# Performance work log

Measured on AMD Instinct MI355X. Metric: run time of the kernel, lower is better.

## Reference

```python
import jax, jax.numpy as jnp
import numpy as np

EPS_BN = 1e-5
EPS_NORM = 1e-12
TEMPERATURE = 0.1
TEMPLATE_LAMBDA = 0.5
KERNEL_WIDTH = 5


def conv1d(x, w, b, pad):
    # x: (B, Cin, W), w: (Cout, Cin, K)
    y = jax.lax.conv_general_dilated(x, w, window_strides=(1,), padding=[(pad, pad)],
                                     dimension_numbers=('NCW', 'OIW', 'NCW'))
    return y + b[None, :, None]


def batchnorm(x, g, be):
    # training-mode BN: batch stats over (B, W), biased variance (as torch)
    m = jnp.mean(x, axis=(0, 2), keepdims=True)
    v = jnp.mean((x - m) ** 2, axis=(0, 2), keepdims=True)
    return g[None, :, None] * (x - m) * jax.lax.rsqrt(v + EPS_BN) + be[None, :, None]


def maxpool4(x):
    return jax.lax.reduce_window(x, -jnp.inf, jax.lax.max, (1, 1, 4), (1, 1, 4), 'VALID')


def adaptive_avg_pool1d(x, k):
    # faithful torch AdaptiveAvgPool1d bin boundaries
    W = x.shape[-1]
    outs = []
    for i in range(k):
        s = (i * W) // k
        e = -(-((i + 1) * W) // k)  # ceil
        outs.append(jnp.mean(x[..., s:e], axis=-1))
    return jnp.stack(outs, axis=-1)


def l2norm(x):
    n = jnp.linalg.norm(x, axis=-1, keepdims=True)
    return x / jnp.maximum(n, EPS_NORM)


def encoder(x, w1, b1, g1, be1, w2, b2, g2, be2, w3, b3, g3, be3):
    h = maxpool4(jax.nn.relu(batchnorm(conv1d(x, w1, b1, 8), g1, be1)))
    h = maxpool4(jax.nn.relu(batchnorm(conv1d(h, w2, b2, 8), g2, be2)))
    h = maxpool4(jax.nn.relu(batchnorm(conv1d(h, w3, b3, 8), g3, be3)))
    return h  # (B, C, W=L/64)


def template_head(h, tw1, tb1, tg1, tbe1, tw2, tb2, tg2, tbe2):
    k = jax.nn.relu(batchnorm(conv1d(h, tw1, tb1, 2), tg1, tbe1))
    k = jax.nn.relu(batchnorm(conv1d(k, tw2, tb2, 1), tg2, tbe2))
    return adaptive_avg_pool1d(k, KERNEL_WIDTH)  # (B, C, W_k)


def template_similarity(k, h):
    # Equivalent to the torch B*B*C grouped 'same' conv1d followed by
    # sum over channels and mean over positions: since the result is the
    # SUM over all output positions of a zero-padded cross-correlation,
    # it factorizes as einsum of k with shifted window-sums of h.
    k = k - jnp.mean(k, axis=-1, keepdims=True)
    k = l2norm(k)  # (B, C, Wk)
    h = h - jnp.mean(h, axis=-1, keepdims=True)
    h = l2norm(h)  # (B, C, W)
    Wk = k.shape[-1]
    W = h.shape[-1]
    pad = (Wk - 1) // 2  # padding='same' for odd kernel
    hp = jnp.pad(h, ((0, 0), (0, 0), (pad, pad)))
    # S[j,c,t] = sum_w hp[j,c,w+t]  for t in [0, Wk)
    S = jnp.stack([jnp.sum(hp[:, :, t:t + W], axis=-1) for t in range(Wk)], axis=-1)
    return jnp.einsum('ick,jck->ij', k, S) / W  # (B, B)


def infonce(sim):
    logp = jax.nn.log_softmax(sim / TEMPERATURE, axis=-1)
    return -jnp.mean(jnp.diagonal(logp))


def template_contrastive_loss(k1, k2):
    B = k1.shape[0]
    a = l2norm(k1.reshape(B, -1))
    b = l2norm(k2.reshape(B, -1))
    return infonce(jnp.matmul(a, b.T) * TEMPERATURE / TEMPERATURE) if False else infonce(jnp.matmul(a, b.T))


def setup_inputs() -> dict:
    key = jax.random.key(0)
    ks = jax.random.split(key, 12)
    B, L, C = 256, 8192, 64
    inp = {
        'x1': jax.random.normal(ks[0], (B, 1, L), dtype=jnp.float32),
        'x2': jax.random.normal(ks[1], (B, 1, L), dtype=jnp.float32),
        # encoder params
        'w1': jax.random.normal(ks[2], (16, 1, 17), dtype=jnp.float32) * 0.1,
        'b1': jnp.zeros((16,), jnp.float32),
        'g1': jnp.ones((16,), jnp.float32), 'be1': jnp.zeros((16,), jnp.float32),
        'w2': jax.random.normal(ks[3], (32, 16, 17), dtype=jnp.float32) * 0.05,
        'b2': jnp.zeros((32,), jnp.float32),
        'g2': jnp.ones((32,), jnp.float32), 'be2': jnp.zeros((32,), jnp.float32),
        'w3': jax.random.normal(ks[4], (C, 32, 17), dtype=jnp.float32) * 0.04,
        'b3': jnp.zeros((C,), jnp.float32),
        'g3': jnp.ones((C,), jnp.float32), 'be3': jnp.zeros((C,), jnp.float32),
        # template head params
        'tw1': jax.random.normal(ks[5], (C, C, 5), dtype=jnp.float32) * 0.05,
        'tb1': jnp.zeros((C,), jnp.float32),
        'tg1': jnp.ones((C,), jnp.float32), 'tbe1': jnp.zeros((C,), jnp.float32),
        'tw2': jax.random.normal(ks[6], (C, C, 3), dtype=jnp.float32) * 0.07,
        'tb2': jnp.zeros((C,), jnp.float32),
        'tg2': jnp.ones((C,), jnp.float32), 'tbe2': jnp.zeros((C,), jnp.float32),
    }
    return inp


def reference(x1, x2, w1, b1, g1, be1, w2, b2, g2, be2, w3, b3, g3, be3,
              tw1, tb1, tg1, tbe1, tw2, tb2, tg2, tbe2):
    enc = (w1, b1, g1, be1, w2, b2, g2, be2, w3, b3, g3, be3)
    th = (tw1, tb1, tg1, tbe1, tw2, tb2, tg2, tbe2)
    h1 = encoder(x1, *enc)
    h2 = encoder(x2, *enc)
    k1 = template_head(h1, *th)
    k2 = template_head(h2, *th)
    loss_matching = (infonce(template_similarity(k1, h2)) +
                     infonce(template_similarity(k2, h1))) / 2
    loss_template = template_contrastive_loss(k1, k2)
    return loss_matching + TEMPLATE_LAMBDA * loss_template
```

## Files before the change

### kernel.cpp

```cpp
#include <hip/hip_runtime.h>
#include <hip/hip_bf16.h>
#include <math.h>


#define BSZ2 512
#define NTHR 256

typedef __attribute__((ext_vector_type(8))) short bf16x8;
typedef __attribute__((ext_vector_type(4))) float f32x4;

static inline int ceil_divll(long long a, int b) { return (int)((a + b - 1) / b); }

__device__ __forceinline__ unsigned short f2bf(float f) {
    unsigned u = __float_as_uint(f);
    u = (u + 0x7FFFu + ((u >> 16) & 1u)) >> 16;
    return (unsigned short)u;
}
__device__ __forceinline__ float bf2f(unsigned short h) {
    return __uint_as_float(((unsigned)h) << 16);
}
__device__ __forceinline__ float bflo(unsigned u) { return __uint_as_float(u << 16); }
__device__ __forceinline__ float bfhi(unsigned u) { return __uint_as_float(u & 0xFFFF0000u); }

template<int WT, int MODE>
__global__ __launch_bounds__(256)
void conv1_mfma(const float* __restrict__ x1, const float* __restrict__ x2,
                const unsigned short* __restrict__ wpack1, const float* __restrict__ bias,
                const float* __restrict__ scale, const float* __restrict__ shift,
                unsigned short* __restrict__ out, float* __restrict__ partials)
{
    constexpr int W = 8192;
    constexpr int CHUNK = 4 * WT * 16;
    __shared__ float xs[CHUNK + 32];
    __shared__ float sred[(MODE == 0) ? 4 : 1][16];
    __shared__ float ssred[(MODE == 0) ? 4 : 1][16];

    const int tid = threadIdx.x;
    const int ntile = W / CHUNK;
    const int b = blockIdx.x / ntile;
    const int w0 = (blockIdx.x % ntile) * CHUNK;
    const float* xrow = (b < 256) ? x1 + (long long)b * W : x2 + (long long)(b - 256) * W;

    for (int i = tid; i < CHUNK + 32; i += 256) {
        const int gw = w0 - 8 + i;
        xs[i] = (gw >= 0 && gw < W) ? xrow[gw] : 0.f;
    }
    __syncthreads();

    const int lane = tid & 63, wave = tid >> 6;
    const int n = lane & 15, kq = lane >> 4;
    const bf16x8 a = *(const bf16x8*)(wpack1 + lane * 8);

    f32x4 acc[WT];
#pragma unroll
    for (int wt = 0; wt < WT; ++wt) { acc[wt][0]=0.f; acc[wt][1]=0.f; acc[wt][2]=0.f; acc[wt][3]=0.f; }

    const int base0 = wave * WT * 16 + n + kq * 8;
#pragma unroll
    for (int wt = 0; wt < WT; ++wt) {
        bf16x8 bv;
#pragma unroll
        for (int j = 0; j < 8; ++j) {
            __hip_bfloat16 h = __float2bfloat16(xs[base0 + wt * 16 + j]);
            bv[j] = *reinterpret_cast<short*>(&h);
        }
        acc[wt] = __builtin_amdgcn_mfma_f32_16x16x32_bf16(bv, a, acc[wt], 0, 0, 0);
    }

    if (MODE == 0) {
        const float bi = bias[n];
        float s_ = 0.f, ss_ = 0.f;
#pragma unroll
        for (int wt = 0; wt < WT; ++wt)
#pragma unroll
            for (int e = 0; e < 4; ++e) {
                const float y = acc[wt][e] + bi;
                s_ += y; ss_ += y * y;
            }
        s_  += __shfl_xor(s_, 16, 64);  s_  += __shfl_xor(s_, 32, 64);
        ss_ += __shfl_xor(ss_, 16, 64); ss_ += __shfl_xor(ss_, 32, 64);
        if (lane < 16) { sred[wave][n] = s_; ssred[wave][n] = ss_; }
        __syncthreads();
        if (tid < 16) {
            float sumv = 0.f, sumsq = 0.f;
#pragma unroll
            for (int wv = 0; wv < 4; ++wv) { sumv += sred[wv][tid]; sumsq += ssred[wv][tid]; }
            partials[((long long)blockIdx.x * 16 + tid) * 2 + 0] = sumv;
            partials[((long long)blockIdx.x * 16 + tid) * 2 + 1] = sumsq;
        }
    } else {
        const int half = b >> 8;
        const float bi = bias[n];
        const float scv = scale[half * 16 + n];
        const float shv = shift[half * 16 + n];
#pragma unroll
        for (int wt = 0; wt < WT; ++wt) {
            float v[4];
#pragma unroll
            for (int e = 0; e < 4; ++e) v[e] = fmaf(scv, acc[wt][e] + bi, shv);
            const float mx = fmaxf(fmaxf(fmaxf(v[0], v[1]), fmaxf(v[2], v[3])), 0.f);
            const int wp = (w0 >> 2) + wave * WT * 4 + wt * 4 + kq;
            out[((long long)b * 2048 + wp) * 16 + n] = f2bf(mx);
        }
    }
}

template<int COUT>
__global__ void finalize2(const float* __restrict__ partials, int nblk_half, float invN,
                          const float* __restrict__ g, const float* __restrict__ be,
                          float* __restrict__ scale, float* __restrict__ shift)
{
    const int co = blockIdx.x;
    const int half = blockIdx.y;
    const float* P = partials + (size_t)half * nblk_half * COUT * 2;
    float s = 0.f, ss = 0.f;
    for (int i = threadIdx.x; i < nblk_half; i += NTHR) {
        s  += P[((long long)i * COUT + co) * 2 + 0];
        ss += P[((long long)i * COUT + co) * 2 + 1];
    }
    __shared__ float red[NTHR][2];
    red[threadIdx.x][0] = s; red[threadIdx.x][1] = ss;
    __syncthreads();
    for (int off = NTHR / 2; off > 0; off >>= 1) {
        if ((int)threadIdx.x < off) {
            red[threadIdx.x][0] += red[threadIdx.x + off][0];
            red[threadIdx.x][1] += red[threadIdx.x + off][1];
        }
        __syncthreads();
    }
    if (threadIdx.x == 0) {
        const float m = red[0][0] * invN;
        const float v = red[0][1] * invN - m * m;
        const float inv = rsqrtf(v + 1e-5f);
        const float sc = g[co] * inv;
        scale[half * COUT + co] = sc;
        shift[half * COUT + co] = be[co] - sc * m;
    }
}

template<int CIN, int KK, int DT, int NP, int S, int CT>
__device__ __forceinline__ void pack_one(int idx, const float* __restrict__ wgt,
                                         unsigned short* __restrict__ wp)
{
    const int j = idx & 7;
    const int l = (idx >> 3) & 63;
    int rest = idx >> 9;
    const int ct = rest % CT; rest /= CT;
    const int s = rest % S;
    const int p = rest / S;
    const int co = ct * 16 + (l & 15);
    const int k = (l >> 4) * 8 + j;
    int ci, t;
    if (DT == 2) { ci = k & (CIN - 1); t = p * 2 + (k >> 4); }
    else         { ci = s * 32 + k;    t = p; }
    float v = (t < KK) ? wgt[((long long)co * CIN + ci) * KK + t] : 0.f;
    wp[idx] = f2bf(v);
}

__global__ void build_all_wpacks(const float* __restrict__ w1, const float* __restrict__ w2,
                                 const float* __restrict__ w3,
                                 const float* __restrict__ tw1, const float* __restrict__ tw2,
                                 unsigned short* __restrict__ wp1,
                                 unsigned short* __restrict__ wp2, unsigned short* __restrict__ wp3,
                                 unsigned short* __restrict__ wpt1, unsigned short* __restrict__ wpt2)
{
    const int idx = blockIdx.x * NTHR + threadIdx.x;
    const int n1 = 512;
    const int n2 = 9 * 1 * 2 * 512;
    const int n3 = 17 * 1 * 4 * 512;
    const int nt1 = 5 * 2 * 4 * 512;
    const int nt2 = 3 * 2 * 4 * 512;
    if (idx < n1) {
        const int j = idx & 7, l = idx >> 3;
        const int co = l & 15, k = (l >> 4) * 8 + j;
        wp1[idx] = f2bf((k < 17) ? w1[co * 17 + k] : 0.f);
    }
    else if (idx < n1 + n2) pack_one<16, 17, 2, 9, 1, 2>(idx - n1, w2, wp2);
    else if (idx < n1 + n2 + n3) pack_one<32, 17, 1, 17, 1, 4>(idx - n1 - n2, w3, wp3);
    else if (idx < n1 + n2 + n3 + nt1) pack_one<64, 5, 1, 5, 2, 4>(idx - n1 - n2 - n3, tw1, wpt1);
    else if (idx < n1 + n2 + n3 + nt1 + nt2) pack_one<64, 3, 1, 3, 2, 4>(idx - n1 - n2 - n3 - nt1, tw2, wpt2);
}

template<int CIN, int COUT, int KK, int PAD, int DT, int NP, int S, int CT, int ST,
         int SRCM, int OUTM>
__global__ __launch_bounds__(256)
void conv_mfma2(const unsigned short* __restrict__ xA, const unsigned short* __restrict__ xB,
                const float* __restrict__ pscale, const float* __restrict__ pshift,
                const unsigned short* __restrict__ wpack, const float* __restrict__ bias,
                unsigned short* __restrict__ outA, unsigned short* __restrict__ outB,
                float* __restrict__ partials, int W)
{
    constexpr int CHUNK = 4 * ST * 16;
    constexpr int ROWB = CIN * 2 + 16;
    constexpr int ROWS = CHUNK + KK + (DT - 1) + 1;
    constexpr int DPR = CIN / 2;
    __shared__ __align__(16) unsigned char lx[ROWS * ROWB];
    __shared__ float sred[4][CT][16];
    __shared__ float ssred[4][CT][16];
    __shared__ float scb[(SRCM > 0) ? CIN : 1];
    __shared__ float shb[(SRCM > 0) ? CIN : 1];

    const int tid = threadIdx.x;
    const int ntile = W / CHUNK;
    const int b = blockIdx.x / ntile;
    const int tile = blockIdx.x % ntile;
    const int w0 = tile * CHUNK;

    if (SRCM > 0) {
        if (tid < CIN) {
            scb[tid] = pscale[(b >> 8) * CIN + tid];
            shb[tid] = pshift[(b >> 8) * CIN + tid];
        }
        __syncthreads();
    }

    for (int d = tid; d < ROWS * DPR; d += 256) {
        const int row = d / DPR;
        const int col = d % DPR;
        const int gw = w0 - PAD + row;
        unsigned v = 0;
        if (gw >= 0 && gw < W) {
            const long long src = ((long long)b * W + gw) * CIN + col * 2;
            if (SRCM == 0) {
                v = *(const unsigned*)(xA + src);
            } else {
                const unsigned va = *(const unsigned*)(xA + src);
                const float sc0 = scb[col * 2], sh0 = shb[col * 2];
                const float sc1 = scb[col * 2 + 1], sh1 = shb[col * 2 + 1];
                float f0, f1;
                if (SRCM == 1) {
                    const unsigned vb = *(const unsigned*)(xB + src);
                    f0 = fmaxf(fmaf(sc0, (sc0 > 0.f) ? bflo(va) : bflo(vb), sh0), 0.f);
                    f1 = fmaxf(fmaf(sc1, (sc1 > 0.f) ? bfhi(va) : bfhi(vb), sh1), 0.f);
                } else {
                    f0 = fmaxf(fmaf(sc0, bflo(va), sh0), 0.f);
                    f1 = fmaxf(fmaf(sc1, bfhi(va), sh1), 0.f);
                }
                v = (unsigned)f2bf(f0) | ((unsigned)f2bf(f1) << 16);
            }
        }
        *(unsigned*)(lx + row * ROWB + col * 4) = v;
    }
    __syncthreads();

    const int lane = tid & 63, wave = tid >> 6;
    const int n = lane & 15, kq = lane >> 4;
    int rowbase, cbyte;
    if (DT == 2) { rowbase = wave * ST * 16 + n + (kq >> 1); cbyte = (kq & 1) * 16; }
    else         { rowbase = wave * ST * 16 + n;             cbyte = kq * 16; }

    f32x4 acc[ST][CT];
#pragma unroll
    for (int st = 0; st < ST; ++st)
#pragma unroll
        for (int ct = 0; ct < CT; ++ct) { acc[st][ct][0]=0.f; acc[st][ct][1]=0.f; acc[st][ct][2]=0.f; acc[st][ct][3]=0.f; }

#pragma unroll
    for (int p = 0; p < NP; ++p) {
#pragma unroll
        for (int s = 0; s < S; ++s) {
            bf16x8 a[CT];
#pragma unroll
            for (int ct = 0; ct < CT; ++ct)
                a[ct] = *(const bf16x8*)(wpack + (((long long)(p * S + s) * CT + ct) * 64 + lane) * 8);
#pragma unroll
            for (int st = 0; st < ST; ++st) {
                const int r = rowbase + st * 16 + p * DT;
                const bf16x8 bf = *(const bf16x8*)(lx + r * ROWB + cbyte + s * 64);
#pragma unroll
                for (int ct = 0; ct < CT; ++ct)
                    acc[st][ct] = __builtin_amdgcn_mfma_f32_16x16x32_bf16(bf, a[ct], acc[st][ct], 0, 0, 0);
            }
        }
    }

    float s_[CT], ss_[CT];
#pragma unroll
    for (int ct = 0; ct < CT; ++ct) { s_[ct] = 0.f; ss_[ct] = 0.f; }

#pragma unroll
    for (int st = 0; st < ST; ++st) {
        const int wbase = w0 + wave * ST * 16 + st * 16 + kq * 4;
#pragma unroll
        for (int ct = 0; ct < CT; ++ct) {
            const float bi = bias[ct * 16 + n];
            float v[4];
#pragma unroll
            for (int e = 0; e < 4; ++e) {
                v[e] = acc[st][ct][e] + bi;
                s_[ct] += v[e];
                ss_[ct] += v[e] * v[e];
            }
            if (OUTM == 0) {
#pragma unroll
                for (int e = 0; e < 4; ++e)
                    outA[((long long)b * W + wbase + e) * COUT + ct * 16 + n] = f2bf(v[e]);
            } else {
                const float mx = fmaxf(fmaxf(v[0], v[1]), fmaxf(v[2], v[3]));
                const float mn = fminf(fminf(v[0], v[1]), fminf(v[2], v[3]));
                const long long o = ((long long)b * (W >> 2) + (wbase >> 2)) * COUT + ct * 16 + n;
                outA[o] = f2bf(mx);
                outB[o] = f2bf(mn);
            }
        }
    }
#pragma unroll
    for (int ct = 0; ct < CT; ++ct) {
        s_[ct]  += __shfl_xor(s_[ct], 16, 64);  s_[ct]  += __shfl_xor(s_[ct], 32, 64);
        ss_[ct] += __shfl_xor(ss_[ct], 16, 64); ss_[ct] += __shfl_xor(ss_[ct], 32, 64);
    }
    if (lane < 16) {
#pragma unroll
        for (int ct = 0; ct < CT; ++ct) { sred[wave][ct][n] = s_[ct]; ssred[wave][ct][n] = ss_[ct]; }
    }
    __syncthreads();
    if (tid < COUT) {
        const int ct = tid >> 4, nn = tid & 15;
        float sumv = 0.f, sumsq = 0.f;
#pragma unroll
        for (int wv = 0; wv < 4; ++wv) { sumv += sred[wv][ct][nn]; sumsq += ssred[wv][ct][nn]; }
        partials[((long long)blockIdx.x * COUT + tid) * 2 + 0] = sumv;
        partials[((long long)blockIdx.x * COUT + tid) * 2 + 1] = sumsq;
    }
}

__global__ void tail_pool_srow(const unsigned short* __restrict__ yT2b,
                               const float* __restrict__ scT2, const float* __restrict__ shT2,
                               const unsigned short* __restrict__ yMax3,
                               const unsigned short* __restrict__ yMin3,
                               const float* __restrict__ scS3, const float* __restrict__ shS3,
                               float* __restrict__ kn, float* __restrict__ ab,
                               float* __restrict__ Sv)
{
    __shared__ float hb[128][64];
    const int tid = threadIdx.x;
    if (blockIdx.x < BSZ2) {
        const int b = blockIdx.x;
        __shared__ float pk[320];
        __shared__ float red2[NTHR];
        const uint2* yd = (const uint2*)(yT2b + (long long)b * 128 * 64);
        for (int i = tid; i < 128 * 16; i += 256) {
            const int w = i >> 4, c4 = (i & 15) * 4;
            const float* scp = scT2 + (b >> 8) * 64 + c4;
            const float* shp = shT2 + (b >> 8) * 64 + c4;
            const uint2 v = yd[i];
            hb[w][c4 + 0] = fmaxf(fmaf(scp[0], bflo(v.x), shp[0]), 0.f);
            hb[w][c4 + 1] = fmaxf(fmaf(scp[1], bfhi(v.x), shp[1]), 0.f);
            hb[w][c4 + 2] = fmaxf(fmaf(scp[2], bflo(v.y), shp[2]), 0.f);
            hb[w][c4 + 3] = fmaxf(fmaf(scp[3], bfhi(v.y), shp[3]), 0.f);
        }
        __syncthreads();
        const int bs[5] = {0, 25, 51, 76, 102};
        const int be[5] = {26, 52, 77, 103, 128};
        for (int o = tid; o < 320; o += 256) {
            const int cc = o & 63, bin = o >> 6;
            float acc = 0.f;
            for (int w = bs[bin]; w < be[bin]; ++w) acc += hb[w][cc];
            pk[cc * 5 + bin] = acc / (float)(be[bin] - bs[bin]);
        }
        __syncthreads();
        float n2p = pk[tid] * pk[tid];
        if (tid < 64) n2p += pk[256 + tid] * pk[256 + tid];
        red2[tid] = n2p;
        __syncthreads();
        for (int off = NTHR / 2; off > 0; off >>= 1) {
            if (tid < off) red2[tid] += red2[tid + off];
            __syncthreads();
        }
        const float nrm = fmaxf(sqrtf(red2[0]), 1e-12f);
        for (int i = tid; i < 320; i += 256) ab[(long long)b * 320 + i] = pk[i] / nrm;
        if (tid < 64) {
            const float* p = pk + tid * 5;
            float m = 0.f;
            for (int t = 0; t < 5; ++t) m += p[t];
            m *= 0.2f;
            float v[5]; float q = 0.f;
            for (int t = 0; t < 5; ++t) { v[t] = p[t] - m; q += v[t] * v[t]; }
            const float n = fmaxf(sqrtf(q), 1e-12f);
            float* o = kn + ((long long)b * 64 + tid) * 5;
            for (int t = 0; t < 5; ++t) o[t] = v[t] / n;
        }
    } else {
        __shared__ float red[4][64];
        __shared__ float mrow[64];
        const int b = blockIdx.x - BSZ2;
        const int c = tid & 63, grp = tid >> 6;
        const uint2* ya = (const uint2*)(yMax3 + (long long)b * 128 * 64);
        const uint2* yb = (const uint2*)(yMin3 + (long long)b * 128 * 64);
        for (int i = tid; i < 128 * 16; i += 256) {
            const int w = i >> 4, c4 = (i & 15) * 4;
            const float* scp = scS3 + (b >> 8) * 64 + c4;
            const float* shp = shS3 + (b >> 8) * 64 + c4;
            const uint2 va = ya[i], vb = yb[i];
            hb[w][c4 + 0] = fmaxf(fmaf(scp[0], (scp[0] > 0.f) ? bflo(va.x) : bflo(vb.x), shp[0]), 0.f);
            hb[w][c4 + 1] = fmaxf(fmaf(scp[1], (scp[1] > 0.f) ? bfhi(va.x) : bfhi(vb.x), shp[1]), 0.f);
            hb[w][c4 + 2] = fmaxf(fmaf(scp[2], (scp[2] > 0.f) ? bflo(va.y) : bflo(vb.y), shp[2]), 0.f);
            hb[w][c4 + 3] = fmaxf(fmaf(scp[3], (scp[3] > 0.f) ? bfhi(va.y) : bfhi(vb.y), shp[3]), 0.f);
        }
        __syncthreads();
        float s = 0.f;
        for (int w = grp * 32; w < grp * 32 + 32; ++w) s += hb[w][c];
        red[grp][c] = s;
        __syncthreads();
        if (tid < 64) mrow[tid] = (red[0][tid] + red[1][tid] + red[2][tid] + red[3][tid]) / 128.f;
        __syncthreads();
        const float m = mrow[c];
        float q = 0.f;
        for (int w = grp * 32; w < grp * 32 + 32; ++w) { const float d = hb[w][c] - m; q += d * d; }
        red[grp][c] = q;
        __syncthreads();
        if (tid < 64) {
            const float n2 = red[0][tid] + red[1][tid] + red[2][tid] + red[3][tid];
            const float n = fmaxf(sqrtf(n2), 1e-12f);
            const float m0 = mrow[tid];
            const float h0 = (hb[0][tid] - m0) / n, h1 = (hb[1][tid] - m0) / n;
            const float hN1 = (hb[127][tid] - m0) / n, hN2 = (hb[126][tid] - m0) / n;
            float* o = Sv + ((long long)b * 64 + tid) * 5;
            o[0] = -(hN2 + hN1); o[1] = -hN1; o[2] = 0.f; o[3] = -h0; o[4] = -(h0 + h1);
        }
    }
}

__global__ void simdot_nce(const float* __restrict__ kn, const float* __restrict__ Sv,
                           const float* __restrict__ ab, float* __restrict__ lp)
{
    const int j = threadIdx.x;
    const int i = blockIdx.x;
    const int z = blockIdx.y;
    const float* a;
    const float* b;
    float coef;
    if (z == 0)      { a = kn + (long long)i * 320;         b = Sv + (long long)(256 + j) * 320; coef = 10.f / 128.f; }
    else if (z == 1) { a = kn + (long long)(256 + i) * 320; b = Sv + (long long)j * 320;         coef = 10.f / 128.f; }
    else             { a = ab + (long long)i * 320;         b = ab + (long long)(256 + j) * 320; coef = 10.f; }
    const float4* a4 = (const float4*)a;
    const float4* b4 = (const float4*)b;
    float acc = 0.f;
#pragma unroll 8
    for (int d = 0; d < 80; ++d) {
        const float4 xv = a4[d], yv = b4[d];
        acc += xv.x * yv.x + xv.y * yv.y + xv.z * yv.z + xv.w * yv.w;
    }
    const float v = acc * coef;

    __shared__ float red[NTHR];
    __shared__ float sdiag;
    if (j == i) sdiag = v;
    red[j] = v;
    __syncthreads();
    for (int off = NTHR / 2; off > 0; off >>= 1) {
        if (j < off) red[j] = fmaxf(red[j], red[j + off]);
        __syncthreads();
    }
    const float mx = red[0];
    __syncthreads();
    red[j] = expf(v - mx);
    __syncthreads();
    for (int off = NTHR / 2; off > 0; off >>= 1) {
        if (j < off) red[j] += red[j + off];
        __syncthreads();
    }
    if (j == 0) lp[z * 256 + i] = sdiag - (mx + logf(red[0]));
}

__global__ void final3(const float* __restrict__ lp, float* __restrict__ out)
{
    __shared__ float red[NTHR];
    const int tid = threadIdx.x;
    float l[3];
    for (int z = 0; z < 3; ++z) {
        red[tid] = lp[z * 256 + tid];
        __syncthreads();
        for (int off = NTHR / 2; off > 0; off >>= 1) {
            if (tid < off) red[tid] += red[tid + off];
            __syncthreads();
        }
        l[z] = red[0];
        __syncthreads();
    }
    if (tid == 0)
        out[0] = 0.5f * (-l[0] / 256.f - l[1] / 256.f) + 0.5f * (-l[2] / 256.f);
}


extern "C" void kernel_launch(void* const* d_in, const int* in_sizes, int n_in,
                              void* d_out, int out_size, void* d_ws, size_t ws_size,
                              hipStream_t stream)
{
    const float* x1  = (const float*)d_in[0];
    const float* x2  = (const float*)d_in[1];
    const float* w1  = (const float*)d_in[2];
    const float* b1  = (const float*)d_in[3];
    const float* g1  = (const float*)d_in[4];
    const float* be1 = (const float*)d_in[5];
    const float* w2  = (const float*)d_in[6];
    const float* b2  = (const float*)d_in[7];
    const float* g2  = (const float*)d_in[8];
    const float* be2 = (const float*)d_in[9];
    const float* w3  = (const float*)d_in[10];
    const float* b3  = (const float*)d_in[11];
    const float* g3  = (const float*)d_in[12];
    const float* be3 = (const float*)d_in[13];
    const float* tw1 = (const float*)d_in[14];
    const float* tb1 = (const float*)d_in[15];
    const float* tg1 = (const float*)d_in[16];
    const float* tbe1= (const float*)d_in[17];
    const float* tw2 = (const float*)d_in[18];
    const float* tb2 = (const float*)d_in[19];
    const float* tg2 = (const float*)d_in[20];
    const float* tbe2= (const float*)d_in[21];
    float* out = (float*)d_out;

    char* ws = (char*)d_ws;
    size_t off = 0;
    auto alloc = [&](size_t bytes) -> void* {
        off = (off + 255) & ~(size_t)255;
        void* p = ws + off;
        off += bytes;
        return p;
    };
    typedef unsigned short u16;
    u16* xT2   = (u16*)alloc((size_t)BSZ2 * 2048 * 16 * 2);
    u16* yMax2 = (u16*)alloc((size_t)BSZ2 * 512 * 32 * 2);
    u16* yMin2 = (u16*)alloc((size_t)BSZ2 * 512 * 32 * 2);
    u16* yMax3 = (u16*)alloc((size_t)BSZ2 * 128 * 64 * 2);
    u16* yMin3 = (u16*)alloc((size_t)BSZ2 * 128 * 64 * 2);
    u16* yT1   = (u16*)alloc((size_t)BSZ2 * 128 * 64 * 2);
    u16* yT2b  = (u16*)alloc((size_t)BSZ2 * 128 * 64 * 2);
    u16* wp1  = (u16*)alloc((size_t)512 * 2);
    u16* wp2  = (u16*)alloc((size_t)9 * 1 * 2 * 512 * 2);
    u16* wp3  = (u16*)alloc((size_t)17 * 1 * 4 * 512 * 2);
    u16* wpt1 = (u16*)alloc((size_t)5 * 2 * 4 * 512 * 2);
    u16* wpt2 = (u16*)alloc((size_t)3 * 2 * 4 * 512 * 2);
    float* kn   = (float*)alloc((size_t)BSZ2 * 320 * 4);
    float* ab   = (float*)alloc((size_t)BSZ2 * 320 * 4);
    float* Sv   = (float*)alloc((size_t)BSZ2 * 320 * 4);
    float* lp   = (float*)alloc((size_t)3 * 256 * 4);
    float* partials = (float*)alloc((size_t)16384 * 16 * 2 * 4);
    float* scales = (float*)alloc((size_t)5 * 128 * 4);
    float* shifts = (float*)alloc((size_t)5 * 128 * 4);
    float* sc1 = scales + 0 * 128, * sh1 = shifts + 0 * 128;
    float* sc2 = scales + 1 * 128, * sh2 = shifts + 1 * 128;
    float* sc3 = scales + 2 * 128, * sh3 = shifts + 2 * 128;
    float* sct1 = scales + 3 * 128, * sht1 = shifts + 3 * 128;
    float* sct2 = scales + 4 * 128, * sht2 = shifts + 4 * 128;

    build_all_wpacks<<<303, NTHR, 0, stream>>>(w1, w2, w3, tw1, tw2, wp1, wp2, wp3, wpt1, wpt2);

    {
        const int nblk = BSZ2 * (8192 / 512);
        conv1_mfma<8, 0><<<nblk, 256, 0, stream>>>(x1, x2, wp1, b1, nullptr, nullptr, nullptr, partials);
        dim3 fg(16, 2);
        finalize2<16><<<fg, NTHR, 0, stream>>>(partials, nblk / 2, 1.f / ((float)256 * 8192), g1, be1, sc1, sh1);
        conv1_mfma<8, 1><<<nblk, 256, 0, stream>>>(x1, x2, wp1, b1, sc1, sh1, xT2, nullptr);
    }
    {
        const int nblk = BSZ2 * (2048 / 512);
        conv_mfma2<16,32,17,8,2,9,1,2,8, 0,1><<<nblk, 256, 0, stream>>>(
            xT2, nullptr, nullptr, nullptr, wp2, b2, yMax2, yMin2, partials, 2048);
        dim3 fg(32, 2);
        finalize2<32><<<fg, NTHR, 0, stream>>>(partials, nblk / 2, 1.f / ((float)256 * 2048), g2, be2, sc2, sh2);
    }
    {
        const int nblk = BSZ2 * (512 / 256);
        conv_mfma2<32,64,17,8,1,17,1,4,4, 1,1><<<nblk, 256, 0, stream>>>(
            yMax2, yMin2, sc2, sh2, wp3, b3, yMax3, yMin3, partials, 512);
        dim3 fg(64, 2);
        finalize2<64><<<fg, NTHR, 0, stream>>>(partials, nblk / 2, 1.f / ((float)256 * 512), g3, be3, sc3, sh3);
    }
    {
        conv_mfma2<64,64,5,2,1,5,2,4,2, 1,0><<<BSZ2, 256, 0, stream>>>(
            yMax3, yMin3, sc3, sh3, wpt1, tb1, yT1, nullptr, partials, 128);
        dim3 fg(64, 2);
        finalize2<64><<<fg, NTHR, 0, stream>>>(partials, 256, 1.f / ((float)256 * 128), tg1, tbe1, sct1, sht1);
    }
    {
        conv_mfma2<64,64,3,1,1,3,2,4,2, 2,0><<<BSZ2, 256, 0, stream>>>(
            yT1, nullptr, sct1, sht1, wpt2, tb2, yT2b, nullptr, partials, 128);
        dim3 fg(64, 2);
        finalize2<64><<<fg, NTHR, 0, stream>>>(partials, 256, 1.f / ((float)256 * 128), tg2, tbe2, sct2, sht2);
    }

    tail_pool_srow<<<2 * BSZ2, 256, 0, stream>>>(yT2b, sct2, sht2, yMax3, yMin3, sc3, sh3, kn, ab, Sv);
    dim3 sg(256, 3);
    simdot_nce<<<sg, NTHR, 0, stream>>>(kn, Sv, ab, lp);
    final3<<<1, NTHR, 0, stream>>>(lp, out);
}
```

Before: 198.0 us.

## Fuse conv1 stats and pooled output into one pass using max/min pooling

The first conv layer previously ran twice: once to gather BatchNorm statistics and once to apply BN, ReLU and maxpool. Now one pass computes the stats and stores both max- and min-pooled pre-BN values in bf16. Conv2 applies the BN affine and ReLU on load, choosing max or min by the sign of the scale, as the later layers already do. This drops the second read of the input and the recomputed conv, but writes two pooled tensors instead of one and makes conv2 read both.

Result: faster. 190.8 us (-3.6%).

```diff
diff --git a/kernel.cpp b/kernel.cpp
--- a/kernel.cpp
+++ b/kernel.cpp
@@ -16,24 +16,21 @@
     u = (u + 0x7FFFu + ((u >> 16) & 1u)) >> 16;
     return (unsigned short)u;
 }
-__device__ __forceinline__ float bf2f(unsigned short h) {
-    return __uint_as_float(((unsigned)h) << 16);
-}
 __device__ __forceinline__ float bflo(unsigned u) { return __uint_as_float(u << 16); }
 __device__ __forceinline__ float bfhi(unsigned u) { return __uint_as_float(u & 0xFFFF0000u); }
 
-template<int WT, int MODE>
+template<int WT>
 __global__ __launch_bounds__(256)
 void conv1_mfma(const float* __restrict__ x1, const float* __restrict__ x2,
                 const unsigned short* __restrict__ wpack1, const float* __restrict__ bias,
-                const float* __restrict__ scale, const float* __restrict__ shift,
-                unsigned short* __restrict__ out, float* __restrict__ partials)
+                unsigned short* __restrict__ outMax, unsigned short* __restrict__ outMin,
+                float* __restrict__ partials)
 {
     constexpr int W = 8192;
     constexpr int CHUNK = 4 * WT * 16;
     __shared__ float xs[CHUNK + 32];
-    __shared__ float sred[(MODE == 0) ? 4 : 1][16];
-    __shared__ float ssred[(MODE == 0) ? 4 : 1][16];
+    __shared__ float sred[4][16];
+    __shared__ float ssred[4][16];
 
     const int tid = threadIdx.x;
     const int ntile = W / CHUNK;
@@ -62,46 +59,37 @@
 #pragma unroll
         for (int j = 0; j < 8; ++j) {
             __hip_bfloat16 h = __float2bfloat16(xs[base0 + wt * 16 + j]);
-            bv[j] = *reinterpret_cast<short*>(&h);
+            bv[j] = *reinterpret_cast<const short*>(&h);
         }
         acc[wt] = __builtin_amdgcn_mfma_f32_16x16x32_bf16(bv, a, acc[wt], 0, 0, 0);
     }
 
-    if (MODE == 0) {
-        const float bi = bias[n];
-        float s_ = 0.f, ss_ = 0.f;
-#pragma unroll
-        for (int wt = 0; wt < WT; ++wt)
-#pragma unroll
-            for (int e = 0; e < 4; ++e) {
-                const float y = acc[wt][e] + bi;
-                s_ += y; ss_ += y * y;
-            }
-        s_  += __shfl_xor(s_, 16, 64);  s_  += __shfl_xor(s_, 32, 64);
-        ss_ += __shfl_xor(ss_, 16, 64); ss_ += __shfl_xor(ss_, 32, 64);
-        if (lane < 16) { sred[wave][n] = s_; ssred[wave][n] = ss_; }
-        __syncthreads();
-        if (tid < 16) {
-            float sumv = 0.f, sumsq = 0.f;
-#pragma unroll
-            for (int wv = 0; wv < 4; ++wv) { sumv += sred[wv][tid]; sumsq += ssred[wv][tid]; }
-            partials[((long long)blockIdx.x * 16 + tid) * 2 + 0] = sumv;
-            partials[((long long)blockIdx.x * 16 + tid) * 2 + 1] = sumsq;
-        }
-    } else {
-        const int half = b >> 8;
-        const float bi = bias[n];
-        const float scv = scale[half * 16 + n];
-        const float shv = shift[half * 16 + n];
-#pragma unroll
-        for (int wt = 0; wt < WT; ++wt) {
-            float v[4];
-#pragma unroll
-            for (int e = 0; e < 4; ++e) v[e] = fmaf(scv, acc[wt][e] + bi, shv);
-            const float mx = fmaxf(fmaxf(fmaxf(v[0], v[1]), fmaxf(v[2], v[3])), 0.f);
-            const int wp = (w0 >> 2) + wave * WT * 4 + wt * 4 + kq;
-            out[((long long)b * 2048 + wp) * 16 + n] = f2bf(mx);
-        }
+    const float bi = bias[n];
+    float s_ = 0.f, ss_ = 0.f;
+#pragma unroll
+    for (int wt = 0; wt < WT; ++wt) {
+        float v[4];
+#pragma unroll
+        for (int e = 0; e < 4; ++e) {
+            v[e] = acc[wt][e] + bi;
+            s_ += v[e]; ss_ += v[e] * v[e];
+        }
+        const float mx = fmaxf(fmaxf(v[0], v[1]), fmaxf(v[2], v[3]));
+        const float mn = fminf(fminf(v[0], v[1]), fminf(v[2], v[3]));
+        const int wp = (w0 >> 2) + wave * WT * 4 + wt * 4 + kq;
+        outMax[((long long)b * 2048 + wp) * 16 + n] = f2bf(mx);
+        outMin[((long long)b * 2048 + wp) * 16 + n] = f2bf(mn);
+    }
+    s_  += __shfl_xor(s_, 16, 64);  s_  += __shfl_xor(s_, 32, 64);
+    ss_ += __shfl_xor(ss_, 16, 64); ss_ += __shfl_xor(ss_, 32, 64);
+    if (lane < 16) { sred[wave][n] = s_; ssred[wave][n] = ss_; }
+    __syncthreads();
+    if (tid < 16) {
+        float sumv = 0.f, sumsq = 0.f;
+#pragma unroll
+        for (int wv = 0; wv < 4; ++wv) { sumv += sred[wv][tid]; sumsq += ssred[wv][tid]; }
+        partials[((long long)blockIdx.x * 16 + tid) * 2 + 0] = sumv;
+        partials[((long long)blockIdx.x * 16 + tid) * 2 + 1] = sumsq;
     }
 }
 
@@ -351,12 +339,12 @@
         }
         __syncthreads();
         const int bs[5] = {0, 25, 51, 76, 102};
-        const int be[5] = {26, 52, 77, 103, 128};
+        const int be5[5] = {26, 52, 77, 103, 128};
         for (int o = tid; o < 320; o += 256) {
             const int cc = o & 63, bin = o >> 6;
             float acc = 0.f;
-            for (int w = bs[bin]; w < be[bin]; ++w) acc += hb[w][cc];
-            pk[cc * 5 + bin] = acc / (float)(be[bin] - bs[bin]);
+            for (int w = bs[bin]; w < be5[bin]; ++w) acc += hb[w][cc];
+            pk[cc * 5 + bin] = acc / (float)(be5[bin] - bs[bin]);
         }
         __syncthreads();
         float n2p = pk[tid] * pk[tid];
@@ -520,7 +508,8 @@
         return p;
     };
     typedef unsigned short u16;
-    u16* xT2   = (u16*)alloc((size_t)BSZ2 * 2048 * 16 * 2);
+    u16* yMax1 = (u16*)alloc((size_t)BSZ2 * 2048 * 16 * 2);
+    u16* yMin1 = (u16*)alloc((size_t)BSZ2 * 2048 * 16 * 2);
     u16* yMax2 = (u16*)alloc((size_t)BSZ2 * 512 * 32 * 2);
     u16* yMin2 = (u16*)alloc((size_t)BSZ2 * 512 * 32 * 2);
     u16* yMax3 = (u16*)alloc((size_t)BSZ2 * 128 * 64 * 2);
@@ -549,36 +538,35 @@
 
     {
         const int nblk = BSZ2 * (8192 / 512);
-        conv1_mfma<8, 0><<<nblk, 256, 0, stream>>>(x1, x2, wp1, b1, nullptr, nullptr, nullptr, partials);
+        conv1_mfma<8><<<nblk, 256, 0, stream>>>(x1, x2, wp1, b1, yMax1, yMin1, partials);
         dim3 fg(16, 2);
-        finalize2<16><<<fg, NTHR, 0, stream>>>(partials, nblk / 2, 1.f / ((float)256 * 8192), g1, be1, sc1, sh1);
-        conv1_mfma<8, 1><<<nblk, 256, 0, stream>>>(x1, x2, wp1, b1, sc1, sh1, xT2, nullptr);
+        finalize2<16><<<fg, NTHR, 0, stream>>>(partials, nblk / 2, 1.f / (256.f * 8192.f), g1, be1, sc1, sh1);
     }
     {
         const int nblk = BSZ2 * (2048 / 512);
-        conv_mfma2<16,32,17,8,2,9,1,2,8, 0,1><<<nblk, 256, 0, stream>>>(
-            xT2, nullptr, nullptr, nullptr, wp2, b2, yMax2, yMin2, partials, 2048);
+        conv_mfma2<16,32,17,8,2,9,1,2,8, 1,1><<<nblk, 256, 0, stream>>>(
+            yMax1, yMin1, sc1, sh1, wp2, b2, yMax2, yMin2, partials, 2048);
         dim3 fg(32, 2);
-        finalize2<32><<<fg, NTHR, 0, stream>>>(partials, nblk / 2, 1.f / ((float)256 * 2048), g2, be2, sc2, sh2);
+        finalize2<32><<<fg, NTHR, 0, stream>>>(partials, nblk / 2, 1.f / (256.f * 2048.f), g2, be2, sc2, sh2);
     }
     {
         const int nblk = BSZ2 * (512 / 256);
         conv_mfma2<32,64,17,8,1,17,1,4,4, 1,1><<<nblk, 256, 0, stream>>>(
             yMax2, yMin2, sc2, sh2, wp3, b3, yMax3, yMin3, partials, 512);
         dim3 fg(64, 2);
-        finalize2<64><<<fg, NTHR, 0, stream>>>(partials, nblk / 2, 1.f / ((float)256 * 512), g3, be3, sc3, sh3);
+        finalize2<64><<<fg, NTHR, 0, stream>>>(partials, nblk / 2, 1.f / (256.f * 512.f), g3, be3, sc3, sh3);
     }
     {
         conv_mfma2<64,64,5,2,1,5,2,4,2, 1,0><<<BSZ2, 256, 0, stream>>>(
             yMax3, yMin3, sc3, sh3, wpt1, tb1, yT1, nullptr, partials, 128);
         dim3 fg(64, 2);
-        finalize2<64><<<fg, NTHR, 0, stream>>>(partials, 256, 1.f / ((float)256 * 128), tg1, tbe1, sct1, sht1);
+        finalize2<64><<<fg, NTHR, 0, stream>>>(partials, 256, 1.f / (256.f * 128.f), tg1, tbe1, sct1, sht1);
     }
     {
         conv_mfma2<64,64,3,1,1,3,2,4,2, 2,0><<<BSZ2, 256, 0, stream>>>(
             yT1, nullptr, sct1, sht1, wpt2, tb2, yT2b, nullptr, partials, 128);
         dim3 fg(64, 2);
-        finalize2<64><<<fg, NTHR, 0, stream>>>(partials, 256, 1.f / ((float)256 * 128), tg2, tbe2, sct2, sht2);
+        finalize2<64><<<fg, NTHR, 0, stream>>>(partials, 256, 1.f / (256.f * 128.f), tg2, tbe2, sct2, sht2);
     }
 
     tail_pool_srow<<<2 * BSZ2, 256, 0, stream>>>(yT2b, sct2, sht2, yMax3, yMin3, sc3, sh3, kn, ab, Sv);
```
